# Kernel tuning notes

Measured on AMD Instinct MI355X. Metric: run time of the kernel, lower is better.

Reference implementation:

```python
import jax, jax.numpy as jnp
import numpy as np

EPS = 1e-5


def _extract3x3(x, stride=1):
    # channel-major patch extraction: output [B, C*9, Ho, Wo], each channel's 3x3 window contiguous
    B, C, H, W = x.shape
    xp = jnp.pad(x, ((0, 0), (0, 0), (1, 1), (1, 1)))
    Ho = (H + 2 - 3) // stride + 1
    Wo = (W + 2 - 3) // stride + 1
    pats = [xp[:, :, i:i + (Ho - 1) * stride + 1:stride, j:j + (Wo - 1) * stride + 1:stride]
            for i in range(3) for j in range(3)]
    return jnp.stack(pats, axis=2).reshape(B, C * 9, Ho, Wo)


def _amm(patches, centroids, lut, inv_temp):
    # patches: [B, D, H, W] channel-major, D = ncodebooks * subvec_len
    # centroids: [ncb, k, sub], lut: [ncb, k, out_channels]
    B, D, H, W = patches.shape
    ncb, k, sub = centroids.shape
    v = patches.reshape(B, ncb, sub, H * W).transpose(0, 3, 1, 2)  # [B, L, ncb, sub]
    # negative squared distance to each codeword (||v||^2 dropped: constant over k)
    scores = 2.0 * jnp.einsum('blcs,cks->blck', v, centroids) - jnp.sum(centroids * centroids, -1)[None, None]
    attn = jax.nn.softmax(scores * inv_temp, axis=-1)          # soft codeword assignment
    out = jnp.einsum('blck,cko->blo', attn, lut)                # LUT gather/sum over codebooks
    return out.transpose(0, 2, 1).reshape(B, -1, H, W)


def _bn(x, g, b):
    m = x.mean((0, 2, 3), keepdims=True)
    v = x.var((0, 2, 3), keepdims=True)
    return g[None, :, None, None] * (x - m) * jax.lax.rsqrt(v + EPS) + b[None, :, None, None]


def setup_inputs() -> dict:
    key = jax.random.key(0)
    ks = jax.random.split(key, 8)
    B, C, H, W = 32, 1024, 14, 14
    width, out_c, K = 256, 1024, 16
    return {
        'x': jax.random.normal(ks[0], (B, C, H, W), jnp.float32),
        'c1_centroids': jax.random.normal(ks[1], (C // 4, K, 4), jnp.float32),
        'c1_lut': jax.random.normal(ks[2], (C // 4, K, width), jnp.float32) * 0.05,
        'c1_invt': jnp.ones((), jnp.float32),
        'c2_centroids': jax.random.normal(ks[3], (width, K, 9), jnp.float32),
        'c2_lut': jax.random.normal(ks[4], (width, K, width), jnp.float32) * 0.05,
        'c2_invt': jnp.ones((), jnp.float32),
        'c3_centroids': jax.random.normal(ks[5], (width // 4, K, 4), jnp.float32),
        'c3_lut': jax.random.normal(ks[6], (width // 4, K, out_c), jnp.float32) * 0.05,
        'c3_invt': jnp.ones((), jnp.float32),
        'bn1_g': jnp.ones((width,), jnp.float32), 'bn1_b': jnp.zeros((width,), jnp.float32),
        'bn2_g': jnp.ones((width,), jnp.float32), 'bn2_b': jnp.zeros((width,), jnp.float32),
        'bn3_g': jnp.ones((out_c,), jnp.float32), 'bn3_b': jnp.zeros((out_c,), jnp.float32),
    }


def reference(x, c1_centroids, c1_lut, c1_invt, c2_centroids, c2_lut, c2_invt,
              c3_centroids, c3_lut, c3_invt, bn1_g, bn1_b, bn2_g, bn2_b, bn3_g, bn3_b):
    identity = x
    out = _amm(x, c1_centroids, c1_lut, c1_invt)                 # amm_conv1x1, stride 1
    out = jax.nn.relu(_bn(out, bn1_g, bn1_b))
    out = _amm(_extract3x3(out, 1), c2_centroids, c2_lut, c2_invt)  # amm_conv3x3, stride 1, pad 1
    out = jax.nn.relu(_bn(out, bn2_g, bn2_b))
    out = _amm(out, c3_centroids, c3_lut, c3_invt)               # amm_conv1x1
    out = _bn(out, bn3_g, bn3_b)
    return jax.nn.relu(out + identity)
```

## Files before the change

kernel.cpp:

```cpp
#include <hip/hip_runtime.h>
#include <hip/hip_bf16.h>

#define EPSV 1e-5f

typedef unsigned short u16;
typedef __attribute__((ext_vector_type(8))) short short8;
typedef __attribute__((ext_vector_type(4))) float f32x4;
typedef __hip_bfloat16 bf16;

__device__ __forceinline__ unsigned int pack2(float a, float b) {
  bf16 ha = __float2bfloat16(a), hb = __float2bfloat16(b);
  u16 ua, ub;
  __builtin_memcpy(&ua, &ha, 2);
  __builtin_memcpy(&ub, &hb, 2);
  return (unsigned int)ua | ((unsigned int)ub << 16);
}

typedef __attribute__((address_space(1))) const void gvoid_t;
typedef __attribute__((address_space(3))) void lvoid_t;
__device__ __forceinline__ void gload16(const void* g, void* l) {
  __builtin_amdgcn_global_load_lds((gvoid_t*)g, (lvoid_t*)l, 16, 0, 0);
}


__global__ __launch_bounds__(256) void prep_kernel(
    const float* __restrict__ x, const float* __restrict__ cent,
    const float* __restrict__ invt, u16* __restrict__ attn,
    const float* __restrict__ s1, bf16* __restrict__ d1,
    const float* __restrict__ s2, bf16* __restrict__ d2,
    const float* __restrict__ s3, bf16* __restrict__ d3)
{
  __shared__ __align__(16) float sh[7012];
  const int tid = threadIdx.x;
  if (blockIdx.x >= 1024) {
    const int bid = blockIdx.x - 1024;
    const int which = bid >> 8, sub = bid & 255;
    const float* in = (which == 0) ? s1 : (which == 1) ? s2 : s3;
    bf16* out = (which == 0) ? d1 : (which == 1) ? d2 : d3;
    const int K = (which == 2) ? 1024 : 4096;
    const int N = (which == 2) ? 1024 : 256;
    const int kt = K >> 6;
    const int bk = sub & (kt - 1), bn = sub / kt;
    const int k0 = bk * 64, n0 = bn * 64;
    float* t = sh;
    for (int idx = tid; idx < 4096; idx += 256) {
      int r = idx >> 6, c = idx & 63;
      t[r * 65 + c] = in[(size_t)(k0 + r) * N + n0 + c];
    }
    __syncthreads();
    for (int idx = tid; idx < 4096; idx += 256) {
      int r = idx >> 6, c = idx & 63;
      out[(size_t)(n0 + r) * K + k0 + c] = __float2bfloat16(t[c * 65 + r]);
    }
    return;
  }
  float* vs = sh;
  float* cs = sh + 6468;
  const int bi = blockIdx.x >> 5, cg = blockIdx.x & 31;
  const float* xb = x + ((size_t)bi * 1024 + cg * 32) * 196;
  for (int e = tid; e < 3136; e += 256) {
    int c = e / 98, p2 = e - c * 98;
    float2 w = *(const float2*)&xb[(size_t)c * 196 + p2 * 2];
    vs[(p2 * 2) * 33 + c] = w.x;
    vs[(p2 * 2 + 1) * 33 + c] = w.y;
  }
  if (tid < 128) {
    int cb = tid >> 4, kk = tid & 15;
    *(float4*)&cs[cb * 68 + kk * 4] =
        *(const float4*)&cent[(size_t)(cg * 8 + cb) * 64 + kk * 4];
  }
  __syncthreads();
  const float it = invt[0];
  const int cbL = tid & 7, pj = tid >> 3;
  float4 cv[16]; float cn[16];
  #pragma unroll
  for (int k = 0; k < 16; k++) {
    cv[k] = *(const float4*)&cs[cbL * 68 + k * 4];
    cn[k] = cv[k].x * cv[k].x + cv[k].y * cv[k].y + cv[k].z * cv[k].z + cv[k].w * cv[k].w;
  }
  for (int p = pj; p < 196; p += 32) {
    const float* vp = &vs[p * 33 + cbL * 4];
    const float v0 = vp[0], v1 = vp[1], v2 = vp[2], v3 = vp[3];
    float s[16], mx = -3e38f;
    #pragma unroll
    for (int k = 0; k < 16; k++) {
      float d = v0 * cv[k].x + v1 * cv[k].y + v2 * cv[k].z + v3 * cv[k].w;
      s[k] = it * (2.f * d - cn[k]);
      mx = fmaxf(mx, s[k]);
    }
    float sum = 0.f;
    #pragma unroll
    for (int k = 0; k < 16; k++) { float e = __expf(s[k] - mx); s[k] = e; sum += e; }
    const float r = 1.f / sum;
    uint4 w0, w1;
    w0.x = pack2(s[0] * r,  s[1] * r);  w0.y = pack2(s[2] * r,  s[3] * r);
    w0.z = pack2(s[4] * r,  s[5] * r);  w0.w = pack2(s[6] * r,  s[7] * r);
    w1.x = pack2(s[8] * r,  s[9] * r);  w1.y = pack2(s[10] * r, s[11] * r);
    w1.z = pack2(s[12] * r, s[13] * r); w1.w = pack2(s[14] * r, s[15] * r);
    uint4* dst = (uint4*)(attn + (size_t)(bi * 196 + p) * 4096 + (cg * 8 + cbL) * 16);
    dst[0] = w0; dst[1] = w1;
  }
}

__global__ __launch_bounds__(256) void attn2_kernel(const float* __restrict__ out1,
    const float* __restrict__ g, const float* __restrict__ bb,
    const float* __restrict__ Sacc, const float* __restrict__ cent,
    const float* __restrict__ invt, u16* __restrict__ attn)
{
  __shared__ float vs[16 * 16 * 16];
  __shared__ __align__(16) float cs[16 * 196];
  __shared__ float cnl[16 * 17];
  __shared__ float ssl[32];
  const int tid = threadIdx.x;
  const int bi = blockIdx.x >> 4, cg = blockIdx.x & 15;
  const float it = invt[0];
  if (tid < 16) {
    const int ch = cg * 16 + tid;
    float S = Sacc[ch], S2 = Sacc[256 + ch];
    float mean = S * (1.f / 6272.f);
    float var = S2 * (1.f / 6272.f) - mean * mean;
    float sc = g[ch] * rsqrtf(var + EPSV);
    ssl[tid] = sc; ssl[16 + tid] = bb[ch] - mean * sc;
  }
  for (int e = tid; e < 4096; e += 256) vs[e] = 0.f;
  const float it2 = 2.f * it;
  for (int idx = tid; idx < 576; idx += 256) {
    int cb = idx / 36, f4i = idx - cb * 36;
    float4 w = *(const float4*)&cent[(size_t)(cg * 16 + cb) * 144 + f4i * 4];
    int j0 = f4i * 4;
    #pragma unroll
    for (int t = 0; t < 4; t++) {
      int j = j0 + t, k = j / 9, jj = j - k * 9;
      cs[cb * 196 + k * 12 + jj] = it2 * ((const float*)&w)[t];
    }
  }
  {
    int cb = tid >> 4, k = tid & 15;
    const float* cc = &cent[(size_t)(cg * 16 + cb) * 144 + k * 9];
    float cn = 0.f;
    #pragma unroll
    for (int j = 0; j < 9; j++) cn = fmaf(cc[j], cc[j], cn);
    cnl[cb * 17 + k] = it * cn;
  }
  __syncthreads();
  for (int e = tid; e < 784; e += 256) {
    int p = e >> 2, c4 = e & 3;
    int r = p / 14, xc = p - r * 14;
    float4 w = *(const float4*)&out1[(size_t)(bi * 196 + p) * 256 + cg * 16 + c4 * 4];
    float* dst = &vs[((r + 1) * 16 + (xc + 1)) * 16 + c4 * 4];
    dst[0] = fmaxf(w.x * ssl[c4 * 4 + 0] + ssl[16 + c4 * 4 + 0], 0.f);
    dst[1] = fmaxf(w.y * ssl[c4 * 4 + 1] + ssl[16 + c4 * 4 + 1], 0.f);
    dst[2] = fmaxf(w.z * ssl[c4 * 4 + 2] + ssl[16 + c4 * 4 + 2], 0.f);
    dst[3] = fmaxf(w.w * ssl[c4 * 4 + 3] + ssl[16 + c4 * 4 + 3], 0.f);
  }
  __syncthreads();
  const int cb = tid & 15, pj = tid >> 4;
  for (int i0 = 0; i0 < 13; i0 += 2) {
    const int p0 = pj + (i0 << 4);
    const int p1 = pj + ((i0 + 1) << 4);
    const int np = (p1 < 196) ? 2 : ((p0 < 196) ? 1 : 0);
    if (np == 0) break;
    float v[2][9];
    #pragma unroll
    for (int i = 0; i < 2; i++) if (i < np) {
      const int p = i ? p1 : p0;
      const int r = p / 14, xc = p - r * 14;
      #pragma unroll
      for (int dy = 0; dy < 3; dy++)
        #pragma unroll
        for (int dx = 0; dx < 3; dx++)
          v[i][dy * 3 + dx] = vs[((r + dy) * 16 + xc + dx) * 16 + cb];
    }
    float s[2][16];
    #pragma unroll
    for (int k = 0; k < 16; k++) {
      const float* ck = &cs[cb * 196 + k * 12];
      const float4 ca = *(const float4*)ck;
      const float4 cbv = *(const float4*)(ck + 4);
      const float c8 = ck[8];
      const float cnv = cnl[cb * 17 + k];
      float c9[9] = {ca.x, ca.y, ca.z, ca.w, cbv.x, cbv.y, cbv.z, cbv.w, c8};
      #pragma unroll
      for (int i = 0; i < 2; i++) if (i < np) {
        float d = -cnv;
        #pragma unroll
        for (int j = 0; j < 9; j++) d = fmaf(c9[j], v[i][j], d);
        s[i][k] = d;
      }
    }
    #pragma unroll
    for (int i = 0; i < 2; i++) if (i < np) {
      const int p = i ? p1 : p0;
      float mx = -3e38f;
      #pragma unroll
      for (int k = 0; k < 16; k++) mx = fmaxf(mx, s[i][k]);
      float sum = 0.f;
      #pragma unroll
      for (int k = 0; k < 16; k++) { float e = __expf(s[i][k] - mx); s[i][k] = e; sum += e; }
      const float r = 1.f / sum;
      uint4 w0, w1;
      w0.x = pack2(s[i][0] * r,  s[i][1] * r);  w0.y = pack2(s[i][2] * r,  s[i][3] * r);
      w0.z = pack2(s[i][4] * r,  s[i][5] * r);  w0.w = pack2(s[i][6] * r,  s[i][7] * r);
      w1.x = pack2(s[i][8] * r,  s[i][9] * r);  w1.y = pack2(s[i][10] * r, s[i][11] * r);
      w1.z = pack2(s[i][12] * r, s[i][13] * r); w1.w = pack2(s[i][14] * r, s[i][15] * r);
      uint4* dst = (uint4*)(attn + (size_t)(bi * 196 + p) * 4096 + (cg * 16 + cb) * 16);
      dst[0] = w0; dst[1] = w1;
    }
  }
}

__global__ __launch_bounds__(256) void attn3_kernel(const float* __restrict__ out2,
    const float* __restrict__ g, const float* __restrict__ bb,
    const float* __restrict__ Sacc, const float* __restrict__ cent,
    const float* __restrict__ invt, bf16* __restrict__ attn)
{
  __shared__ float ssl[512];
  const int t = threadIdx.x;
  {
    float S = Sacc[t], S2 = Sacc[256 + t];
    float mean = S * (1.f / 6272.f);
    float var = S2 * (1.f / 6272.f) - mean * mean;
    float sc = g[t] * rsqrtf(var + EPSV);
    ssl[t] = sc; ssl[256 + t] = bb[t] - mean * sc;
  }
  __syncthreads();
  const int cb = t & 63, ml = t >> 6;
  const int m0 = blockIdx.x * 16;
  const float it = invt[0];
  float4 cv[16]; float cn[16];
  const float4* cc = (const float4*)(cent + cb * 64);
  #pragma unroll
  for (int k = 0; k < 16; k++) {
    cv[k] = cc[k];
    cn[k] = cv[k].x * cv[k].x + cv[k].y * cv[k].y + cv[k].z * cv[k].z + cv[k].w * cv[k].w;
  }
  const float4 scv = *(const float4*)(ssl + cb * 4);
  const float4 shv = *(const float4*)(ssl + 256 + cb * 4);
  for (int gi = 0; gi < 4; gi++) {
    const int m = m0 + gi * 4 + ml;
    float4 xv = *(const float4*)(out2 + (size_t)m * 256 + cb * 4);
    float4 v;
    v.x = fmaxf(xv.x * scv.x + shv.x, 0.f);
    v.y = fmaxf(xv.y * scv.y + shv.y, 0.f);
    v.z = fmaxf(xv.z * scv.z + shv.z, 0.f);
    v.w = fmaxf(xv.w * scv.w + shv.w, 0.f);
    float s[16], mx = -3e38f;
    #pragma unroll
    for (int k = 0; k < 16; k++) {
      float d = v.x * cv[k].x + v.y * cv[k].y + v.z * cv[k].z + v.w * cv[k].w;
      s[k] = it * (2.f * d - cn[k]);
      mx = fmaxf(mx, s[k]);
    }
    float sum = 0.f;
    #pragma unroll
    for (int k = 0; k < 16; k++) { float e = __expf(s[k] - mx); s[k] = e; sum += e; }
    float r = 1.f / sum;
    #pragma unroll
    for (int k = 0; k < 16; k++)
      attn[(size_t)m * 1024 + cb * 16 + k] = __float2bfloat16(s[k] * r);
  }
}

template<int KDIM, int NT, int KSLICES, int BM, int BK>
__global__ __launch_bounds__(512) void gemm_kernel(const u16* __restrict__ A,
    const u16* __restrict__ Bt, float* __restrict__ C, size_t cstride,
    float* __restrict__ zacc, int zn, float* __restrict__ stats)
{
  constexpr int NDIM = NT * 128;
  constexpr int KS = KDIM / KSLICES;
  constexpr int MT = 6272 / BM;
  constexpr int FM = BM / 64;
  constexpr int KU = BK / 32;
  constexpr int SLOTS = BK / 8;
  constexpr int RPC = 64 / SLOTS;
  constexpr int ACALLS = BM / (RPC * 8);
  constexpr int BCALLS = 128 / (RPC * 8);
  __shared__ __align__(16) u16 Asm[2][BM * BK];
  __shared__ __align__(16) u16 Bsm[2][128 * BK];
  const int tid = threadIdx.x;
  if (blockIdx.x == 0 && zacc) {
    for (int i = tid; i < zn; i += 512) zacc[i] = 0.f;
  }
  const int nwg = gridDim.x;
  int wg = blockIdx.x;
  if ((nwg & 7) == 0) wg = (blockIdx.x & 7) * (nwg >> 3) + (blockIdx.x >> 3);
  const int nt = wg % NT;
  const int mt = (wg / NT) % MT;
  const int sl = wg / (NT * MT);
  const int kbeg = sl * KS, kend = kbeg + KS;
  const int m0 = mt * BM, n0 = nt * 128;
  const int lane = tid & 63, wid = tid >> 6;
  const int wm = wid >> 1, wn = wid & 1;
  const int lr = lane / SLOTS, sslot = lane % SLOTS;
  const int gs = sslot ^ (lr & 7);

  f32x4 acc[FM][4];
  #pragma unroll
  for (int i = 0; i < FM; i++)
    #pragma unroll
    for (int j = 0; j < 4; j++) acc[i][j] = (f32x4){0.f, 0.f, 0.f, 0.f};

  const u16* Abase = A + (size_t)m0 * KDIM;
  const u16* Bbase = Bt + (size_t)n0 * KDIM;

  auto stage = [&](int bf, int kb) {
    #pragma unroll
    for (int c = 0; c < ACALLS; c++) {
      const int r0 = (wid * ACALLS + c) * RPC;
      gload16(Abase + (size_t)(r0 + lr) * KDIM + kb + gs * 8, &Asm[bf][r0 * BK]);
    }
    #pragma unroll
    for (int c = 0; c < BCALLS; c++) {
      const int r0 = (wid * BCALLS + c) * RPC;
      gload16(Bbase + (size_t)(r0 + lr) * KDIM + kb + gs * 8, &Bsm[bf][r0 * BK]);
    }
  };

  auto compute = [&](int bf) {
    #pragma unroll
    for (int ks = 0; ks < KU; ks++) {
      short8 a[FM], b[4];
      #pragma unroll
      for (int f = 0; f < FM; f++) {
        const int ra = wm * (BM / 4) + f * 16 + (lane & 15);
        const int ja = (ks * 4 + (lane >> 4)) ^ (ra & 7);
        a[f] = *(const short8*)(&Asm[bf][ra * BK + ja * 8]);
      }
      #pragma unroll
      for (int f = 0; f < 4; f++) {
        const int rb = wn * 64 + f * 16 + (lane & 15);
        const int jb = (ks * 4 + (lane >> 4)) ^ (rb & 7);
        b[f] = *(const short8*)(&Bsm[bf][rb * BK + jb * 8]);
      }
      #pragma unroll
      for (int fm = 0; fm < FM; fm++)
        #pragma unroll
        for (int fn = 0; fn < 4; fn++)
          acc[fm][fn] = __builtin_amdgcn_mfma_f32_16x16x32_bf16(a[fm], b[fn], acc[fm][fn], 0, 0, 0);
    }
  };

  stage(0, kbeg);
  __syncthreads();
  int cur = 0;
  for (int kb = kbeg + BK; kb < kend; kb += BK) {
    stage(cur ^ 1, kb);
    compute(cur);
    __syncthreads();
    cur ^= 1;
  }
  compute(cur);

  float* __restrict__ Cs = C + (size_t)sl * cstride;
  #pragma unroll
  for (int fm = 0; fm < FM; fm++)
    #pragma unroll
    for (int fn = 0; fn < 4; fn++) {
      const int col = n0 + wn * 64 + fn * 16 + (lane & 15);
      const int rbase = m0 + wm * (BM / 4) + fm * 16 + (lane >> 4) * 4;
      #pragma unroll
      for (int r = 0; r < 4; r++)
        Cs[(size_t)(rbase + r) * NDIM + col] = acc[fm][fn][r];
    }

  if (stats) {
    __syncthreads();
    float* red = (float*)&Asm[0][0];
    #pragma unroll
    for (int fn = 0; fn < 4; fn++) {
      float s = 0.f, s2 = 0.f;
      #pragma unroll
      for (int fm = 0; fm < FM; fm++)
        #pragma unroll
        for (int r = 0; r < 4; r++) {
          float v = acc[fm][fn][r];
          s += v; s2 = fmaf(v, v, s2);
        }
      s += __shfl_xor(s, 16);  s += __shfl_xor(s, 32);
      s2 += __shfl_xor(s2, 16); s2 += __shfl_xor(s2, 32);
      if ((lane >> 4) == 0) {
        const int colL = wn * 64 + fn * 16 + (lane & 15);
        red[wm * 256 + colL] = s;
        red[wm * 256 + 128 + colL] = s2;
      }
    }
    __syncthreads();
    if (tid < 256) {
      const int colL = tid & 127, st = (tid >> 7) & 1;
      float v = red[st * 128 + colL] + red[256 + st * 128 + colL]
              + red[512 + st * 128 + colL] + red[768 + st * 128 + colL];
      atomicAdd(&stats[(size_t)st * NDIM + n0 + colL], v);
    }
  }
}

template<int CH, int NBLK, int NSUM>
__global__ __launch_bounds__(256) void bnpart_kernel(const float* __restrict__ buf,
    float* __restrict__ sum_out, float* __restrict__ acc)
{
  constexpr int PC = CH / 256;
  constexpr int ROWS = 6272 / NBLK;
  constexpr size_t PSTR = 6272ull * CH;
  const int t = threadIdx.x, m0 = blockIdx.x * ROWS;
  float s[PC], s2[PC];
  #pragma unroll
  for (int j = 0; j < PC; j++) { s[j] = 0.f; s2[j] = 0.f; }
  for (int i = 0; i < ROWS; i++) {
    const size_t ro = (size_t)(m0 + i) * CH;
    #pragma unroll
    for (int j = 0; j < PC; j++) {
      float v = buf[ro + t + j * 256];
      #pragma unroll
      for (int n = 1; n < NSUM; n++) v += buf[(size_t)n * PSTR + ro + t + j * 256];
      if (NSUM > 1) sum_out[ro + t + j * 256] = v;
      s[j] += v; s2[j] = fmaf(v, v, s2[j]);
    }
  }
  #pragma unroll
  for (int j = 0; j < PC; j++) {
    atomicAdd(&acc[t + j * 256], s[j]);
    atomicAdd(&acc[CH + t + j * 256], s2[j]);
  }
}

__global__ __launch_bounds__(256) void tfinal_kernel(const float* __restrict__ out3,
    const float* __restrict__ g, const float* __restrict__ bb,
    const float* __restrict__ Sacc, const float* __restrict__ x,
    float* __restrict__ out)
{
  __shared__ float t[64 * 199];
  __shared__ float ssl[128];
  const int b = blockIdx.x >> 4, n0 = (blockIdx.x & 15) * 64;
  if (threadIdx.x < 64) {
    const int ch = n0 + threadIdx.x;
    float S = Sacc[ch], S2 = Sacc[1024 + ch];
    float mean = S * (1.f / 6272.f);
    float var = S2 * (1.f / 6272.f) - mean * mean;
    float sc = g[ch] * rsqrtf(var + EPSV);
    ssl[threadIdx.x] = sc; ssl[64 + threadIdx.x] = bb[ch] - mean * sc;
  }
  __syncthreads();
  for (int idx = threadIdx.x; idx < 196 * 64; idx += 256) {
    int p = idx >> 6, ni = idx & 63;
    float v = out3[(size_t)(b * 196 + p) * 1024 + n0 + ni] * ssl[ni] + ssl[64 + ni];
    t[ni * 199 + p] = v;
  }
  __syncthreads();
  for (int idx = threadIdx.x; idx < 64 * 196; idx += 256) {
    int ni = idx / 196, p = idx - ni * 196;
    size_t o = (size_t)(b * 1024 + n0 + ni) * 196 + p;
    out[o] = fmaxf(t[ni * 199 + p] + x[o], 0.f);
  }
}


template<int CIN, int OUT, bool APPLY_BN>
__global__ __launch_bounds__(256) void amm1x1_kernel(
    const float* __restrict__ xin, const float* __restrict__ ss,
    const float* __restrict__ cent, const float* __restrict__ lut,
    const float* __restrict__ invt, float* __restrict__ outbuf)
{
  constexpr int NCB = CIN / 4;
  constexpr int NO = OUT / 256;
  __shared__ float vsm[CIN * 14];
  __shared__ __align__(16) float attn_sm[14 * 16];
  const int tid = threadIdx.x;
  const int b = blockIdx.x / 14, y = blockIdx.x % 14;
  const int rowbase = y * 14;
  for (int e = tid; e < CIN * 14; e += 256) {
    int c = e / 14, xc = e - c * 14;
    float v = xin[(b * CIN + c) * 196 + rowbase + xc];
    if (APPLY_BN) v = fmaxf(v * ss[c] + ss[CIN + c], 0.f);
    vsm[e] = v;
  }
  __syncthreads();
  float acc[14 * NO];
  #pragma unroll
  for (int i = 0; i < 14 * NO; i++) acc[i] = 0.f;
  const float it = invt[0];
  const int p_ = tid >> 4, k_ = tid & 15;
  for (int cb = 0; cb < NCB; ++cb) {
    if (tid < 224) {
      const float* cc = cent + (cb * 16 + k_) * 4;
      float s = 0.f;
      #pragma unroll
      for (int si = 0; si < 4; si++) {
        float cv = cc[si];
        float vv = vsm[(cb * 4 + si) * 14 + p_];
        s = fmaf(cv, 2.f * vv - cv, s);
      }
      s *= it;
      float m = s;
      #pragma unroll
      for (int off = 8; off; off >>= 1) m = fmaxf(m, __shfl_xor(m, off, 16));
      float e = __expf(s - m);
      float sum = e;
      #pragma unroll
      for (int off = 8; off; off >>= 1) sum += __shfl_xor(sum, off, 16);
      attn_sm[p_ * 16 + k_] = e / sum;
    }
    __syncthreads();
    float lv[NO][16];
    #pragma unroll
    for (int j = 0; j < NO; j++)
      #pragma unroll
      for (int k = 0; k < 16; k++)
        lv[j][k] = lut[(cb * 16 + k) * OUT + j * 256 + tid];
    const float4* a4 = (const float4*)attn_sm;
    #pragma unroll
    for (int p = 0; p < 14; p++) {
      float4 q0 = a4[p*4+0], q1 = a4[p*4+1], q2 = a4[p*4+2], q3 = a4[p*4+3];
      float av[16] = {q0.x,q0.y,q0.z,q0.w, q1.x,q1.y,q1.z,q1.w,
                      q2.x,q2.y,q2.z,q2.w, q3.x,q3.y,q3.z,q3.w};
      #pragma unroll
      for (int j = 0; j < NO; j++) {
        float s = acc[p * NO + j];
        #pragma unroll
        for (int k = 0; k < 16; k++) s = fmaf(av[k], lv[j][k], s);
        acc[p * NO + j] = s;
      }
    }
    __syncthreads();
  }
  #pragma unroll
  for (int j = 0; j < NO; j++) {
    int o = j * 256 + tid;
    #pragma unroll
    for (int p = 0; p < 14; p++)
      outbuf[(b * OUT + o) * 196 + rowbase + p] = acc[p * NO + j];
  }
}

__global__ __launch_bounds__(256) void amm3x3_kernel(
    const float* __restrict__ xin, const float* __restrict__ ss,
    const float* __restrict__ cent, const float* __restrict__ lut,
    const float* __restrict__ invt, float* __restrict__ outbuf)
{
  __shared__ float vsm[256 * 3 * 16];
  __shared__ __align__(16) float attn_sm[14 * 16];
  const int tid = threadIdx.x;
  const int b = blockIdx.x / 14, y = blockIdx.x % 14;
  for (int e = tid; e < 256 * 3 * 16; e += 256) {
    int c = e / 48, rem = e - c * 48, i = rem >> 4, col = rem & 15;
    int yy = y + i - 1, xx = col - 1;
    float v = 0.f;
    if (yy >= 0 && yy < 14 && xx >= 0 && xx < 14) {
      v = xin[(b * 256 + c) * 196 + yy * 14 + xx];
      v = fmaxf(v * ss[c] + ss[256 + c], 0.f);
    }
    vsm[e] = v;
  }
  __syncthreads();
  float acc[14];
  #pragma unroll
  for (int i = 0; i < 14; i++) acc[i] = 0.f;
  const float it = invt[0];
  const int p_ = tid >> 4, k_ = tid & 15;
  for (int cb = 0; cb < 256; ++cb) {
    if (tid < 224) {
      const float* cc = cent + (cb * 16 + k_) * 9;
      float s = 0.f;
      #pragma unroll
      for (int i = 0; i < 3; i++)
        #pragma unroll
        for (int j = 0; j < 3; j++) {
          float cv = cc[i * 3 + j];
          float vv = vsm[(cb * 3 + i) * 16 + p_ + j];
          s = fmaf(cv, 2.f * vv - cv, s);
        }
      s *= it;
      float m = s;
      #pragma unroll
      for (int off = 8; off; off >>= 1) m = fmaxf(m, __shfl_xor(m, off, 16));
      float e = __expf(s - m);
      float sum = e;
      #pragma unroll
      for (int off = 8; off; off >>= 1) sum += __shfl_xor(sum, off, 16);
      attn_sm[p_ * 16 + k_] = e / sum;
    }
    __syncthreads();
    float lv[16];
    #pragma unroll
    for (int k = 0; k < 16; k++) lv[k] = lut[(cb * 16 + k) * 256 + tid];
    const float4* a4 = (const float4*)attn_sm;
    #pragma unroll
    for (int p = 0; p < 14; p++) {
      float4 q0 = a4[p*4+0], q1 = a4[p*4+1], q2 = a4[p*4+2], q3 = a4[p*4+3];
      float av[16] = {q0.x,q0.y,q0.z,q0.w, q1.x,q1.y,q1.z,q1.w,
                      q2.x,q2.y,q2.z,q2.w, q3.x,q3.y,q3.z,q3.w};
      float s = acc[p];
      #pragma unroll
      for (int k = 0; k < 16; k++) s = fmaf(av[k], lv[k], s);
      acc[p] = s;
    }
    __syncthreads();
  }
  #pragma unroll
  for (int p = 0; p < 14; p++)
    outbuf[(b * 256 + tid) * 196 + y * 14 + p] = acc[p];
}

template<int CH>
__global__ __launch_bounds__(256) void bnstats_kernel(const float* __restrict__ buf,
    const float* __restrict__ g, const float* __restrict__ bb, float* __restrict__ ss)
{
  const int c = blockIdx.x, tid = threadIdx.x;
  float s = 0.f, s2 = 0.f;
  for (int e = tid; e < 32 * 196; e += 256) {
    int bi = e / 196, l = e - bi * 196;
    float v = buf[(bi * CH + c) * 196 + l];
    s += v; s2 = fmaf(v, v, s2);
  }
  #pragma unroll
  for (int off = 32; off; off >>= 1) { s += __shfl_down(s, off); s2 += __shfl_down(s2, off); }
  __shared__ float red[8];
  int w = tid >> 6;
  if ((tid & 63) == 0) { red[w] = s; red[4 + w] = s2; }
  __syncthreads();
  if (tid == 0) {
    float S  = red[0] + red[1] + red[2] + red[3];
    float S2 = red[4] + red[5] + red[6] + red[7];
    float mean = S * (1.f / 6272.f);
    float var  = S2 * (1.f / 6272.f) - mean * mean;
    float sc = g[c] * rsqrtf(var + EPSV);
    ss[c] = sc;
    ss[CH + c] = bb[c] - mean * sc;
  }
}

__global__ __launch_bounds__(256) void final_old_kernel(float* __restrict__ out3,
    const float* __restrict__ ss, const float* __restrict__ x)
{
  const int total = 32 * 1024 * 196;
  for (int idx = blockIdx.x * 256 + threadIdx.x; idx < total; idx += gridDim.x * 256) {
    int c = (idx / 196) & 1023;
    float v = out3[idx] * ss[c] + ss[1024 + c] + x[idx];
    out3[idx] = fmaxf(v, 0.f);
  }
}


extern "C" void kernel_launch(void* const* d_in, const int* in_sizes, int n_in,
                              void* d_out, int out_size, void* d_ws, size_t ws_size,
                              hipStream_t stream) {
  const float* x   = (const float*)d_in[0];
  const float* c1c = (const float*)d_in[1];
  const float* c1l = (const float*)d_in[2];
  const float* c1t = (const float*)d_in[3];
  const float* c2c = (const float*)d_in[4];
  const float* c2l = (const float*)d_in[5];
  const float* c2t = (const float*)d_in[6];
  const float* c3c = (const float*)d_in[7];
  const float* c3l = (const float*)d_in[8];
  const float* c3t = (const float*)d_in[9];
  const float* g1  = (const float*)d_in[10];
  const float* b1  = (const float*)d_in[11];
  const float* g2  = (const float*)d_in[12];
  const float* b2  = (const float*)d_in[13];
  const float* g3  = (const float*)d_in[14];
  const float* b3  = (const float*)d_in[15];

  float* ws = (float*)d_ws;
  const size_t FAST_NEED = 24255488ull * 4ull;

  if (ws_size >= FAST_NEED) {
    u16*   attnB = (u16*)ws;
    float* partC = ws + 12845056;
    float* out1  = partC + 6422528;
    float* out2  = out1 + 1605632;
    bf16*  lutT1 = (bf16*)(out2 + 1605632);
    bf16*  lutT2 = lutT1 + 1048576;
    bf16*  lutT3 = lutT2 + 1048576;
    float* acc1  = (float*)(lutT3 + 1048576);
    float* acc2  = acc1 + 512;
    float* acc3  = acc2 + 512;
    float* out3  = partC;
    const size_t PART_STRIDE = 1605632;

    prep_kernel<<<1792, 256, 0, stream>>>(x, c1c, c1t, attnB,
                                          c1l, lutT1, c2l, lutT2, c3l, lutT3);

    gemm_kernel<4096, 2, 4, 128, 64><<<392, 512, 0, stream>>>(
        attnB, (const u16*)lutT1, partC, PART_STRIDE, acc1, 512, nullptr);
    bnpart_kernel<256, 196, 4><<<196, 256, 0, stream>>>(partC, out1, acc1);

    attn2_kernel<<<512, 256, 0, stream>>>(out1, g1, b1, acc1, c2c, c2t, attnB);
    gemm_kernel<4096, 2, 4, 128, 64><<<392, 512, 0, stream>>>(
        attnB, (const u16*)lutT2, partC, PART_STRIDE, acc2, 2560, nullptr);
    bnpart_kernel<256, 196, 4><<<196, 256, 0, stream>>>(partC, out2, acc2);

    attn3_kernel<<<392, 256, 0, stream>>>(out2, g2, b2, acc2, c3c, c3t, (bf16*)attnB);
    gemm_kernel<1024, 8, 1, 128, 64><<<392, 512, 0, stream>>>(
        attnB, (const u16*)lutT3, out3, 0, nullptr, 0, acc3);

    tfinal_kernel<<<512, 256, 0, stream>>>(out3, g3, b3, acc3, x, (float*)d_out);
  } else {
    float* out3 = (float*)d_out;
    float* out1 = ws;
    float* out2 = out1 + 32 * 256 * 196;
    float* ss1  = out2 + 32 * 256 * 196;
    float* ss2  = ss1 + 512;
    float* ss3  = ss2 + 512;

    amm1x1_kernel<1024, 256, false><<<448, 256, 0, stream>>>(x, nullptr, c1c, c1l, c1t, out1);
    bnstats_kernel<256><<<256, 256, 0, stream>>>(out1, g1, b1, ss1);
    amm3x3_kernel<<<448, 256, 0, stream>>>(out1, ss1, c2c, c2l, c2t, out2);
    bnstats_kernel<256><<<256, 256, 0, stream>>>(out2, g2, b2, ss2);
    amm1x1_kernel<256, 1024, true><<<448, 256, 0, stream>>>(out2, ss2, c3c, c3l, c3t, out3);
    bnstats_kernel<1024><<<1024, 256, 0, stream>>>(out3, g3, b3, ss3);
    final_old_kernel<<<2048, 256, 0, stream>>>(out3, ss3, x);
  }
}
```

Before: 264.0 us.

## Replace split-K GEMMs with narrow-N full-K tiles and fused BN stats

```diff
diff --git a/kernel.cpp b/kernel.cpp
--- a/kernel.cpp
+++ b/kernel.cpp
@@ -28,10 +28,15 @@
     const float* __restrict__ invt, u16* __restrict__ attn,
     const float* __restrict__ s1, bf16* __restrict__ d1,
     const float* __restrict__ s2, bf16* __restrict__ d2,
-    const float* __restrict__ s3, bf16* __restrict__ d3)
+    const float* __restrict__ s3, bf16* __restrict__ d3,
+    float* __restrict__ accz)
 {
   __shared__ __align__(16) float sh[7012];
   const int tid = threadIdx.x;
+  if (blockIdx.x == 1792) {
+    for (int i = tid; i < 3072; i += 256) accz[i] = 0.f;
+    return;
+  }
   if (blockIdx.x >= 1024) {
     const int bid = blockIdx.x - 1024;
     const int which = bid >> 8, sub = bid & 255;
@@ -261,44 +266,40 @@
   }
 }
 
-template<int KDIM, int NT, int KSLICES, int BM, int BK>
+template<int KDIM, int NDIM, int BM, int BN, int BK>
 __global__ __launch_bounds__(512) void gemm_kernel(const u16* __restrict__ A,
-    const u16* __restrict__ Bt, float* __restrict__ C, size_t cstride,
-    float* __restrict__ zacc, int zn, float* __restrict__ stats)
-{
-  constexpr int NDIM = NT * 128;
-  constexpr int KS = KDIM / KSLICES;
+    const u16* __restrict__ Bt, float* __restrict__ C, float* __restrict__ stats)
+{
+  constexpr int NTL = NDIM / BN;
   constexpr int MT = 6272 / BM;
   constexpr int FM = BM / 64;
+  constexpr int FN = BN / 32;
   constexpr int KU = BK / 32;
   constexpr int SLOTS = BK / 8;
   constexpr int RPC = 64 / SLOTS;
   constexpr int ACALLS = BM / (RPC * 8);
-  constexpr int BCALLS = 128 / (RPC * 8);
+  constexpr int BCALLS = BN / (RPC * 8) ? BN / (RPC * 8) : 1;
+  constexpr int BROWS_PER_WAVE = BN / 8;
   __shared__ __align__(16) u16 Asm[2][BM * BK];
-  __shared__ __align__(16) u16 Bsm[2][128 * BK];
+  __shared__ __align__(16) u16 Bsm[2][BN * BK];
   const int tid = threadIdx.x;
-  if (blockIdx.x == 0 && zacc) {
-    for (int i = tid; i < zn; i += 512) zacc[i] = 0.f;
-  }
-  const int nwg = gridDim.x;
-  int wg = blockIdx.x;
-  if ((nwg & 7) == 0) wg = (blockIdx.x & 7) * (nwg >> 3) + (blockIdx.x >> 3);
-  const int nt = wg % NT;
-  const int mt = (wg / NT) % MT;
-  const int sl = wg / (NT * MT);
-  const int kbeg = sl * KS, kend = kbeg + KS;
-  const int m0 = mt * BM, n0 = nt * 128;
+  const int nwg = MT * NTL;
+  const int xcd = blockIdx.x & 7, base = blockIdx.x >> 3;
+  const int q = nwg >> 3, r = nwg & 7;
+  const int wg = (xcd < r ? xcd * (q + 1) : r * (q + 1) + (xcd - r) * q) + base;
+  const int nt = wg % NTL;
+  const int mt = wg / NTL;
+  const int m0 = mt * BM, n0 = nt * BN;
   const int lane = tid & 63, wid = tid >> 6;
   const int wm = wid >> 1, wn = wid & 1;
   const int lr = lane / SLOTS, sslot = lane % SLOTS;
   const int gs = sslot ^ (lr & 7);
 
-  f32x4 acc[FM][4];
+  f32x4 acc[FM][FN];
   #pragma unroll
   for (int i = 0; i < FM; i++)
     #pragma unroll
-    for (int j = 0; j < 4; j++) acc[i][j] = (f32x4){0.f, 0.f, 0.f, 0.f};
+    for (int j = 0; j < FN; j++) acc[i][j] = (f32x4){0.f, 0.f, 0.f, 0.f};
 
   const u16* Abase = A + (size_t)m0 * KDIM;
   const u16* Bbase = Bt + (size_t)n0 * KDIM;
@@ -312,14 +313,15 @@
     #pragma unroll
     for (int c = 0; c < BCALLS; c++) {
       const int r0 = (wid * BCALLS + c) * RPC;
-      gload16(Bbase + (size_t)(r0 + lr) * KDIM + kb + gs * 8, &Bsm[bf][r0 * BK]);
+      if (r0 < BN)
+        gload16(Bbase + (size_t)(r0 + lr) * KDIM + kb + gs * 8, &Bsm[bf][r0 * BK]);
     }
   };
 
   auto compute = [&](int bf) {
     #pragma unroll
     for (int ks = 0; ks < KU; ks++) {
-      short8 a[FM], b[4];
+      short8 a[FM], b[FN];
       #pragma unroll
       for (int f = 0; f < FM; f++) {
         const int ra = wm * (BM / 4) + f * 16 + (lane & 15);
@@ -327,23 +329,23 @@
         a[f] = *(const short8*)(&Asm[bf][ra * BK + ja * 8]);
       }
       #pragma unroll
-      for (int f = 0; f < 4; f++) {
-        const int rb = wn * 64 + f * 16 + (lane & 15);
+      for (int f = 0; f < FN; f++) {
+        const int rb = wn * (BN / 2) + f * 16 + (lane & 15);
         const int jb = (ks * 4 + (lane >> 4)) ^ (rb & 7);
         b[f] = *(const short8*)(&Bsm[bf][rb * BK + jb * 8]);
       }
       #pragma unroll
       for (int fm = 0; fm < FM; fm++)
         #pragma unroll
-        for (int fn = 0; fn < 4; fn++)
+        for (int fn = 0; fn < FN; fn++)
           acc[fm][fn] = __builtin_amdgcn_mfma_f32_16x16x32_bf16(a[fm], b[fn], acc[fm][fn], 0, 0, 0);
     }
   };
 
-  stage(0, kbeg);
+  stage(0, 0);
   __syncthreads();
   int cur = 0;
-  for (int kb = kbeg + BK; kb < kend; kb += BK) {
+  for (int kb = BK; kb < KDIM; kb += BK) {
     stage(cur ^ 1, kb);
     compute(cur);
     __syncthreads();
@@ -351,75 +353,45 @@
   }
   compute(cur);
 
-  float* __restrict__ Cs = C + (size_t)sl * cstride;
   #pragma unroll
   for (int fm = 0; fm < FM; fm++)
     #pragma unroll
-    for (int fn = 0; fn < 4; fn++) {
-      const int col = n0 + wn * 64 + fn * 16 + (lane & 15);
+    for (int fn = 0; fn < FN; fn++) {
+      const int col = n0 + wn * (BN / 2) + fn * 16 + (lane & 15);
       const int rbase = m0 + wm * (BM / 4) + fm * 16 + (lane >> 4) * 4;
       #pragma unroll
-      for (int r = 0; r < 4; r++)
-        Cs[(size_t)(rbase + r) * NDIM + col] = acc[fm][fn][r];
-    }
-
-  if (stats) {
+      for (int r2 = 0; r2 < 4; r2++)
+        C[(size_t)(rbase + r2) * NDIM + col] = acc[fm][fn][r2];
+    }
+
+  {
     __syncthreads();
     float* red = (float*)&Asm[0][0];
     #pragma unroll
-    for (int fn = 0; fn < 4; fn++) {
+    for (int fn = 0; fn < FN; fn++) {
       float s = 0.f, s2 = 0.f;
       #pragma unroll
       for (int fm = 0; fm < FM; fm++)
         #pragma unroll
-        for (int r = 0; r < 4; r++) {
-          float v = acc[fm][fn][r];
+        for (int r2 = 0; r2 < 4; r2++) {
+          float v = acc[fm][fn][r2];
           s += v; s2 = fmaf(v, v, s2);
         }
       s += __shfl_xor(s, 16);  s += __shfl_xor(s, 32);
       s2 += __shfl_xor(s2, 16); s2 += __shfl_xor(s2, 32);
       if ((lane >> 4) == 0) {
-        const int colL = wn * 64 + fn * 16 + (lane & 15);
-        red[wm * 256 + colL] = s;
-        red[wm * 256 + 128 + colL] = s2;
+        const int colL = wn * (BN / 2) + fn * 16 + (lane & 15);
+        red[wm * (2 * BN) + colL] = s;
+        red[wm * (2 * BN) + BN + colL] = s2;
       }
     }
     __syncthreads();
-    if (tid < 256) {
-      const int colL = tid & 127, st = (tid >> 7) & 1;
-      float v = red[st * 128 + colL] + red[256 + st * 128 + colL]
-              + red[512 + st * 128 + colL] + red[768 + st * 128 + colL];
+    if (tid < 2 * BN) {
+      const int colL = tid % BN, st = tid / BN;
+      float v = red[st * BN + colL] + red[2 * BN + st * BN + colL]
+              + red[4 * BN + st * BN + colL] + red[6 * BN + st * BN + colL];
       atomicAdd(&stats[(size_t)st * NDIM + n0 + colL], v);
     }
-  }
-}
-
-template<int CH, int NBLK, int NSUM>
-__global__ __launch_bounds__(256) void bnpart_kernel(const float* __restrict__ buf,
-    float* __restrict__ sum_out, float* __restrict__ acc)
-{
-  constexpr int PC = CH / 256;
-  constexpr int ROWS = 6272 / NBLK;
-  constexpr size_t PSTR = 6272ull * CH;
-  const int t = threadIdx.x, m0 = blockIdx.x * ROWS;
-  float s[PC], s2[PC];
-  #pragma unroll
-  for (int j = 0; j < PC; j++) { s[j] = 0.f; s2[j] = 0.f; }
-  for (int i = 0; i < ROWS; i++) {
-    const size_t ro = (size_t)(m0 + i) * CH;
-    #pragma unroll
-    for (int j = 0; j < PC; j++) {
-      float v = buf[ro + t + j * 256];
-      #pragma unroll
-      for (int n = 1; n < NSUM; n++) v += buf[(size_t)n * PSTR + ro + t + j * 256];
-      if (NSUM > 1) sum_out[ro + t + j * 256] = v;
-      s[j] += v; s2[j] = fmaf(v, v, s2[j]);
-    }
-  }
-  #pragma unroll
-  for (int j = 0; j < PC; j++) {
-    atomicAdd(&acc[t + j * 256], s[j]);
-    atomicAdd(&acc[CH + t + j * 256], s2[j]);
   }
 }
 
@@ -665,8 +637,8 @@
 
   if (ws_size >= FAST_NEED) {
     u16*   attnB = (u16*)ws;
-    float* partC = ws + 12845056;
-    float* out1  = partC + 6422528;
+    float* out3  = ws + 12845056;
+    float* out1  = out3 + 6422528;
     float* out2  = out1 + 1605632;
     bf16*  lutT1 = (bf16*)(out2 + 1605632);
     bf16*  lutT2 = lutT1 + 1048576;
@@ -674,24 +646,20 @@
     float* acc1  = (float*)(lutT3 + 1048576);
     float* acc2  = acc1 + 512;
     float* acc3  = acc2 + 512;
-    float* out3  = partC;
-    const size_t PART_STRIDE = 1605632;
-
-    prep_kernel<<<1792, 256, 0, stream>>>(x, c1c, c1t, attnB,
-                                          c1l, lutT1, c2l, lutT2, c3l, lutT3);
-
-    gemm_kernel<4096, 2, 4, 128, 64><<<392, 512, 0, stream>>>(
-        attnB, (const u16*)lutT1, partC, PART_STRIDE, acc1, 512, nullptr);
-    bnpart_kernel<256, 196, 4><<<196, 256, 0, stream>>>(partC, out1, acc1);
+
+    prep_kernel<<<1793, 256, 0, stream>>>(x, c1c, c1t, attnB,
+                                          c1l, lutT1, c2l, lutT2, c3l, lutT3, acc1);
+
+    gemm_kernel<4096, 256, 128, 64, 64><<<196, 512, 0, stream>>>(
+        attnB, (const u16*)lutT1, out1, acc1);
 
     attn2_kernel<<<512, 256, 0, stream>>>(out1, g1, b1, acc1, c2c, c2t, attnB);
-    gemm_kernel<4096, 2, 4, 128, 64><<<392, 512, 0, stream>>>(
-        attnB, (const u16*)lutT2, partC, PART_STRIDE, acc2, 2560, nullptr);
-    bnpart_kernel<256, 196, 4><<<196, 256, 0, stream>>>(partC, out2, acc2);
+    gemm_kernel<4096, 256, 128, 64, 64><<<196, 512, 0, stream>>>(
+        attnB, (const u16*)lutT2, out2, acc2);
 
     attn3_kernel<<<392, 256, 0, stream>>>(out2, g2, b2, acc2, c3c, c3t, (bf16*)attnB);
-    gemm_kernel<1024, 8, 1, 128, 64><<<392, 512, 0, stream>>>(
-        attnB, (const u16*)lutT3, out3, 0, nullptr, 0, acc3);
+    gemm_kernel<1024, 1024, 128, 128, 64><<<392, 512, 0, stream>>>(
+        attnB, (const u16*)lutT3, out3, acc3);
 
     tfinal_kernel<<<512, 256, 0, stream>>>(out3, g3, b3, acc3, x, (float*)d_out);
   } else {
```

New measurement: 290.6 us. 1.1x slower.
